# Performance work log

Hardware: AMD Instinct MI355X
Metric: run time of the kernel (lower is better)

The kernel has to match this reference:

```python
import jax, jax.numpy as jnp
import numpy as np

B = 4096
L = 15          # self.length
NINP = 256      # emb_size
NHID = 512      # hidden_size
VOCAB = 30005
TOPK = 10
K = 4 * TOPK + 2   # 42 actions
N_SPLIT = 2 * TOPK
N_STEP = 5      # num_edits
PAD = 30003


def _lstm_dir(x, Wih, Whh, b, reverse):
    # x: [T,B,D]; Wih: [4H,D]; Whh: [4H,H]; b: [4H] (b_ih+b_hh). PyTorch gate order i,f,g,o.
    Bsz, H = x.shape[1], Whh.shape[1]
    def step(carry, xt):
        h, c = carry
        z = xt @ Wih.T + h @ Whh.T + b
        i, f, g, o = jnp.split(z, 4, axis=-1)
        c = jax.nn.sigmoid(f) * c + jax.nn.sigmoid(i) * jnp.tanh(g)
        h = jax.nn.sigmoid(o) * jnp.tanh(c)
        return (h, c), h
    h0 = jnp.zeros((Bsz, H), x.dtype)
    _, ys = jax.lax.scan(step, (h0, h0), x, reverse=reverse)
    return ys  # [T,B,H], position-aligned for both directions


def bilstm(x, Wih0, Whh0, b0, Wih1, Whh1, b1):
    # x: [B,T,D] -> [B,T,2H]; 2-layer bidirectional, zero initial state (matches c0/h0 zeros).
    xt = jnp.swapaxes(x, 0, 1)
    for Wih, Whh, b in ((Wih0, Whh0, b0), (Wih1, Whh1, b1)):
        fw = _lstm_dir(xt, Wih[0], Whh[0], b[0], False)
        bw = _lstm_dir(xt, Wih[1], Whh[1], b[1], True)
        xt = jnp.concatenate([fw, bw], axis=-1)
    return jnp.swapaxes(xt, 0, 1)


def policy_step(st_1, length_t, pos, emb0, key_pos, rep_words, valid_id,
                emb_table, enc_table, Wih0, Whh0, b0, Wih1, Whh1, b1,
                del_vec, hold_vec, mlp_W, mlp_b, mlp1_W, mlp1_b):
    Bsz = st_1.shape[0]
    pos_row = jnp.zeros((L,), jnp.float32).at[pos].set(1.0)         # static pos
    pos_tensor = jnp.broadcast_to(pos_row[None, :, None], (Bsz, L, 1))
    embt = emb_table[st_1] * (1.0 - pos_tensor)
    x = jnp.concatenate([embt, emb0, pos_tensor], axis=2)            # [B,L,2*ninp+1]
    out = bilstm(x, Wih0, Whh0, b0, Wih1, Whh1, b1)                  # [B,L,2*nhid]
    pooled = out[:, pos, :]
    representation = jnp.concatenate(
        [pooled, key_pos[:, pos:pos + 1], jnp.broadcast_to(pos_row[None, :], (Bsz, L))], axis=1)
    # external encoder output is detached in the original
    word_emb = jax.lax.stop_gradient(enc_table[rep_words])           # [B,4*topk,ninp]
    emb2 = jnp.concatenate([word_emb,
                            jnp.broadcast_to(del_vec, (Bsz, 1, NINP)),
                            jnp.broadcast_to(hold_vec, (Bsz, 1, NINP))], axis=1)  # [B,K,ninp]
    onehot = jnp.broadcast_to(jnp.eye(K, dtype=jnp.float32)[None], (Bsz, K, K))
    emb2 = jnp.concatenate([emb2, onehot], axis=2)                   # [B,K,ninp+K]
    rep100 = representation @ mlp_W.T + mlp_b                        # [B,100]
    emb100 = emb2 @ mlp1_W.T + mlp1_b                                # [B,K,100]
    score = jnp.einsum('bkd,bd->bk', emb100, rep100)
    policy = jax.nn.softmax(score, axis=1)
    action = jnp.argmax(policy, axis=1, keepdims=True).astype(jnp.int32)  # eval mode
    pi = jnp.take_along_axis(policy, action, axis=1)                 # [B,1]

    rep_b = (action < N_SPLIT).astype(jnp.int32)
    replaceflag = rep_b * valid_id
    ins_b = ((action >= N_SPLIT) & (action < 2 * N_SPLIT)).astype(jnp.int32)
    insertflag = ins_b * valid_id * (length_t + ins_b <= 15).astype(jnp.int32)
    del_b = (action == 2 * N_SPLIT).astype(jnp.int32)
    deleteflag = del_b * valid_id * (length_t - del_b > 2).astype(jnp.int32)
    holdflag = 1 - replaceflag - insertflag - deleteflag

    action_words = jnp.take_along_axis(rep_words, jnp.clip(action, 0, N_SPLIT - 1), axis=1)  # [B,1]
    rep_seq = jnp.concatenate([action_words, st_1[:, pos + 1:]], axis=1)
    ins_seq = jnp.concatenate([action_words, st_1[:, pos:-1]], axis=1)
    padding = jnp.full((Bsz, 1), PAD, dtype=st_1.dtype)
    del_seq = jnp.concatenate([st_1[:, pos + 1:], padding], axis=1)
    hol_seq = st_1[:, pos:]
    new_tail = (rep_seq * replaceflag + ins_seq * insertflag
                + del_seq * deleteflag + hol_seq * holdflag)
    st = st_1.at[:, pos:].set(new_tail)
    length_tt = insertflag + length_t - deleteflag
    return st, pi, action.astype(jnp.float32), length_tt


def setup_inputs() -> dict:
    key = jax.random.key(0)
    ks = jax.random.split(key, 20)
    s = 0.05
    in0 = 2 * NINP + 1
    in1 = 2 * NHID
    inp = {
        'input_ids': jax.random.randint(ks[0], (B, L), 0, 30000, dtype=jnp.int32),
        'key_pos': jax.random.uniform(ks[1], (B, L), dtype=jnp.float32),
        'sequence_length': jax.random.randint(ks[2], (B, 1), 3, 16, dtype=jnp.int32),
        'rep_words_all': jax.random.randint(ks[3], (B, N_STEP, 4 * TOPK), 0, 30000, dtype=jnp.int32),
        'valid_id_all': jax.random.randint(ks[4], (B, N_STEP, 1), 0, 2, dtype=jnp.int32),
        'emb_table': jax.random.normal(ks[5], (VOCAB, NINP), jnp.float32) * s,
        'enc_table': jax.random.normal(ks[6], (VOCAB, NINP), jnp.float32) * s,
        'Wih0': jax.random.normal(ks[7], (2, 4 * NHID, in0), jnp.float32) * s,
        'Whh0': jax.random.normal(ks[8], (2, 4 * NHID, NHID), jnp.float32) * s,
        'b0': jax.random.normal(ks[9], (2, 4 * NHID), jnp.float32) * s,
        'Wih1': jax.random.normal(ks[10], (2, 4 * NHID, in1), jnp.float32) * s,
        'Whh1': jax.random.normal(ks[11], (2, 4 * NHID, NHID), jnp.float32) * s,
        'b1': jax.random.normal(ks[12], (2, 4 * NHID), jnp.float32) * s,
        'del_vec': jax.random.uniform(ks[13], (1, 1, NINP), dtype=jnp.float32),
        'hold_vec': jax.random.uniform(ks[14], (1, 1, NINP), dtype=jnp.float32),
        'mlp_W': jax.random.normal(ks[15], (100, 2 * NHID + 1 + L), jnp.float32) * s,
        'mlp_b': jnp.zeros((100,), jnp.float32),
        'mlp1_W': jax.random.normal(ks[16], (100, NINP + K), jnp.float32) * s,
        'mlp1_b': jnp.zeros((100,), jnp.float32),
    }
    return inp


def reference(input_ids, key_pos, sequence_length, rep_words_all, valid_id_all,
              emb_table, enc_table, Wih0, Whh0, b0, Wih1, Whh1, b1,
              del_vec, hold_vec, mlp_W, mlp_b, mlp1_W, mlp1_b):
    st = input_ids
    emb0 = emb_table[input_ids]            # embedding of s0, computed once
    length_t = sequence_length
    pis, acts = [], []
    for i in range(N_STEP):
        pos = i % (L - 3) + 2              # static per unrolled step
        st, pi, a, length_t = policy_step(
            st, length_t, pos, emb0, key_pos,
            rep_words_all[:, i, :], valid_id_all[:, i, :],
            emb_table, enc_table, Wih0, Whh0, b0, Wih1, Whh1, b1,
            del_vec, hold_vec, mlp_W, mlp_b, mlp1_W, mlp1_b)
        pis.append(pi)
        acts.append(a)
    pis = jnp.concatenate(pis, axis=1)     # [B,N_STEP]
    actions = jnp.concatenate(acts, axis=1)
    return pis, actions, st, length_t
```

## Files before the change

### kernel.cpp

```cpp
#include <hip/hip_runtime.h>

#define B_ 4096
#define L_ 15
#define NSTEP_ 5
#define VOC_ 30005
#define PAD_ 30003

typedef _Float16 f16;
typedef f16  f16x8 __attribute__((ext_vector_type(8)));
typedef float f32x16 __attribute__((ext_vector_type(16)));

__device__ __forceinline__ float sigf(float x){ return 1.0f/(1.0f+expf(-x)); }

#define MFMA_(d,a,b) d = __builtin_amdgcn_mfma_f32_32x32x16_f16(a,b,d,0,0,0)

struct RecParams {
  const f16 *A1h_0,*A1l_0,*A1h_1,*A1l_1;
  const f16 *A2h_0,*A2l_0,*A2h_1,*A2l_1;
  const f16 *Wfh_0,*Wfl_0,*Wfh_1,*Wfl_1;
  const float *bias_0,*bias_1;
  const f16 *embH,*embL;
  const int *st,*ids;
  float *c_0,*c_1,*h2_0,*h2_1;
  f16 *hh_0,*hl_0,*hh_1,*hl_1;
  int lda1, lda2, ldh, ldh2, k1p, k2p, first, gather, t_0, t_1, pos, b0c, act0, act1;
};

__device__ __forceinline__ int swz(int row, int s){
  int u = ((row&7)<<1) | s;
  return ((row>>3)<<8) + ((u ^ (u>>1))<<4);
}

__global__ __launch_bounds__(256,2) void rec_gemm(RecParams p){
  const int id  = blockIdx.x;
  const int ct4 = id & 15;
  const int dir = (id >> 4) & 1;
  if (!(dir ? p.act1 : p.act0)) return;
  const f16* A1h = dir ? p.A1h_1 : p.A1h_0;
  const f16* A1l = dir ? p.A1l_1 : p.A1l_0;
  const f16* A2h = dir ? p.A2h_1 : p.A2h_0;
  const f16* A2l = dir ? p.A2l_1 : p.A2l_0;
  const f16* Wfh = dir ? p.Wfh_1 : p.Wfh_0;
  const f16* Wfl = dir ? p.Wfl_1 : p.Wfl_0;
  const float* bias = dir ? p.bias_1 : p.bias_0;
  float* cbuf = dir ? p.c_1 : p.c_0;
  float* h2   = dir ? p.h2_1 : p.h2_0;
  f16* hhb = dir ? p.hh_1 : p.hh_0;
  f16* hlb = dir ? p.hl_1 : p.hl_0;
  const int tcur = dir ? p.t_1 : p.t_0;

  const int tid  = threadIdx.x;
  const int lane = tid & 63;
  const int w    = tid >> 6;
  const int mbase = (id >> 5) * 128;

  __shared__ union {
    float z[128*128];
    f16   stg[8][2048];
  } sm;

  f32x16 accM[2][2], accX[2][2];
#pragma unroll
  for (int i=0;i<2;i++)
#pragma unroll
    for (int j=0;j<2;j++)
#pragma unroll
      for (int r=0;r<16;r++){ accM[i][j][r]=0.f; accX[i][j][r]=0.f; }

  const int arow = (w&1)*64 + (lane&31);
  const int fs = lane>>5;
  const int aoff0 = swz(arow,    fs), aoff1 = swz(arow+32, fs);

  const int ct0 = ct4*4 + (w>>1)*2;
  const f16* WfhL = Wfh + (size_t)lane*8;
  const f16* WflL = Wfl + (size_t)lane*8;

  const int srow = tid >> 1, ss = tid & 1;
  const int sws = swz(srow, ss);
  const int ktot = p.k1p + p.k2p;

  int tokT=0, tokI=0, zflag=0;
  if (p.gather){
    int gb = p.b0c + mbase + srow;
    tokT = p.st [gb*L_ + tcur];
    tokI = p.ids[gb*L_ + tcur];
    zflag = (tcur == p.pos) ? 1 : 0;
  }

  f16x8 ra_h0, ra_l0, ra_h1, ra_l1;
  const f16x8 zero8 = {0,0,0,0,0,0,0,0};

  auto gload = [&](int ph){
    if (ph >= ktot) return;
    if (ph < p.k1p){
      if (p.gather){
        if (ph < 8){
          if (zflag){ ra_h0=zero8; ra_l0=zero8; ra_h1=zero8; ra_l1=zero8; }
          else {
            size_t base = (size_t)tokT*256 + ph*32 + ss*8;
            ra_h0 = *(const f16x8*)(p.embH + base);
            ra_l0 = *(const f16x8*)(p.embL + base);
            ra_h1 = *(const f16x8*)(p.embH + base + 16);
            ra_l1 = *(const f16x8*)(p.embL + base + 16);
          }
        } else if (ph < 16){
          size_t base = (size_t)tokI*256 + (ph-8)*32 + ss*8;
          ra_h0 = *(const f16x8*)(p.embH + base);
          ra_l0 = *(const f16x8*)(p.embL + base);
          ra_h1 = *(const f16x8*)(p.embH + base + 16);
          ra_l1 = *(const f16x8*)(p.embL + base + 16);
        } else {
          ra_h0 = zero8; ra_l0 = zero8; ra_h1 = zero8; ra_l1 = zero8;
          if (ss == 0) ra_h0[0] = zflag ? (f16)1.0f : (f16)0.0f;
        }
      } else {
        long base = (long)(mbase+srow)*p.lda1 + ph*32 + ss*8;
        ra_h0 = *(const f16x8*)(A1h + base);
        ra_l0 = *(const f16x8*)(A1l + base);
        ra_h1 = *(const f16x8*)(A1h + base + 16);
        ra_l1 = *(const f16x8*)(A1l + base + 16);
      }
    } else {
      long base = (long)(mbase+srow)*p.lda2 + (ph - p.k1p)*32 + ss*8;
      ra_h0 = *(const f16x8*)(A2h + base);
      ra_l0 = *(const f16x8*)(A2l + base);
      ra_h1 = *(const f16x8*)(A2h + base + 16);
      ra_l1 = *(const f16x8*)(A2l + base + 16);
    }
  };
  auto swrite = [&](int buf){
    *(f16x8*)((char*)sm.stg[buf*4+0] + sws) = ra_h0;
    *(f16x8*)((char*)sm.stg[buf*4+1] + sws) = ra_l0;
    *(f16x8*)((char*)sm.stg[buf*4+2] + sws) = ra_h1;
    *(f16x8*)((char*)sm.stg[buf*4+3] + sws) = ra_l1;
  };

  gload(0); swrite(0); gload(1);
  __syncthreads();

  for (int ph=0; ph<ktot; ++ph){
    const int cur = ph & 1;
    size_t base0 = ((size_t)(ph*2+0)*64 + ct0)*512;
    size_t base1 = ((size_t)(ph*2+1)*64 + ct0)*512;
    f16x8 rbh00 = *(const f16x8*)(WfhL + base0);
    f16x8 rbh01 = *(const f16x8*)(WfhL + base0 + 512);
    f16x8 rbl00 = *(const f16x8*)(WflL + base0);
    f16x8 rbl01 = *(const f16x8*)(WflL + base0 + 512);
    f16x8 rbh10 = *(const f16x8*)(WfhL + base1);
    f16x8 rbh11 = *(const f16x8*)(WfhL + base1 + 512);
    f16x8 rbl10 = *(const f16x8*)(WflL + base1);
    f16x8 rbl11 = *(const f16x8*)(WflL + base1 + 512);
    const char* s0h = (const char*)sm.stg[cur*4+0];
    const char* s0l = (const char*)sm.stg[cur*4+1];
    const char* s1h = (const char*)sm.stg[cur*4+2];
    const char* s1l = (const char*)sm.stg[cur*4+3];
    f16x8 a00h = *(const f16x8*)(s0h + aoff0);
    f16x8 a01h = *(const f16x8*)(s0h + aoff1);
    f16x8 a00l = *(const f16x8*)(s0l + aoff0);
    f16x8 a01l = *(const f16x8*)(s0l + aoff1);
    f16x8 a10h = *(const f16x8*)(s1h + aoff0);
    f16x8 a11h = *(const f16x8*)(s1h + aoff1);
    f16x8 a10l = *(const f16x8*)(s1l + aoff0);
    f16x8 a11l = *(const f16x8*)(s1l + aoff1);
    if (ph+1 < ktot){ swrite((ph+1)&1); gload(ph+2); }
    MFMA_(accM[0][0], a00h, rbh00); MFMA_(accX[0][0], a00h, rbl00); MFMA_(accX[0][0], a00l, rbh00);
    MFMA_(accM[1][0], a01h, rbh00); MFMA_(accX[1][0], a01h, rbl00); MFMA_(accX[1][0], a01l, rbh00);
    MFMA_(accM[0][1], a00h, rbh01); MFMA_(accX[0][1], a00h, rbl01); MFMA_(accX[0][1], a00l, rbh01);
    MFMA_(accM[1][1], a01h, rbh01); MFMA_(accX[1][1], a01h, rbl01); MFMA_(accX[1][1], a01l, rbh01);
    MFMA_(accM[0][0], a10h, rbh10); MFMA_(accX[0][0], a10h, rbl10); MFMA_(accX[0][0], a10l, rbh10);
    MFMA_(accM[1][0], a11h, rbh10); MFMA_(accX[1][0], a11h, rbl10); MFMA_(accX[1][0], a11l, rbh10);
    MFMA_(accM[0][1], a10h, rbh11); MFMA_(accX[0][1], a10h, rbl11); MFMA_(accX[0][1], a10l, rbh11);
    MFMA_(accM[1][1], a11h, rbh11); MFMA_(accX[1][1], a11h, rbl11); MFMA_(accX[1][1], a11l, rbh11);
    __syncthreads();
  }

#pragma unroll
  for (int tm=0;tm<2;tm++)
#pragma unroll
   for (int tn=0;tn<2;tn++){
    int lcol = (w>>1)*64 + tn*32 + (lane&31);
    float bv = bias[ct4*128 + lcol];
#pragma unroll
    for (int r=0;r<16;r++){
      int lrow = (w&1)*64 + tm*32 + (r&3) + 8*(r>>2) + 4*(lane>>5);
      sm.z[lrow*128 + lcol] = accM[tm][tn][r] + 0.000244140625f*accX[tm][tn][r] + bv;
    }
   }
  __syncthreads();

  const int nb = ct4*32;
#pragma unroll
  for (int it=0; it<16; ++it){
    int idx = it*256 + tid;
    int nq = idx & 31, row = idx >> 5;
    float4 g4 = *(const float4*)&sm.z[row*128 + nq*4];
    int m = mbase + row, n = nb + nq;
    float cp = p.first ? 0.f : cbuf[(size_t)m*512 + n];
    float cc = sigf(g4.y)*cp + sigf(g4.x)*tanhf(g4.z);
    float hv = sigf(g4.w)*tanhf(cc);
    cbuf[(size_t)m*512 + n] = cc;
    f16 hi = (f16)hv;
    f16 lo = (f16)((hv - (float)hi)*4096.0f);
    hhb[(size_t)m*p.ldh + n] = hi;
    hlb[(size_t)m*p.ldh + n] = lo;
    if (h2) h2[(size_t)m*p.ldh2 + n] = hv;
  }
}

__global__ void prep_w0(const float* Wih, const float* Whh, const float* b0,
                        f16* Wfh, f16* Wfl, float* bp){
  int gid = blockIdx.x*blockDim.x + threadIdx.x;
  const int PER_DIR = 66*64*64*8;
  if (gid >= 2*PER_DIR) return;
  int dir = gid / PER_DIR;
  int rem = gid % PER_DIR;
  int j = rem & 7, lane = (rem>>3)&63, ct = (rem>>9)&63, kt16 = rem>>15;
  int n4g = ct*32 + (lane&31);
  int n = n4g>>2, g = n4g&3;
  int srow = dir*2048 + g*512 + n;
  int k = kt16*16 + ((lane>>5)<<3) + j;
  float v;
  if (k < 513)       v = Wih[(size_t)srow*513 + k];
  else if (k < 544)  v = 0.f;
  else               v = Whh[(size_t)srow*512 + (k-544)];
  f16 hi = (f16)v;
  Wfh[gid] = hi;
  Wfl[gid] = (f16)((v - (float)hi)*4096.0f);
  if (kt16==0 && (lane>>5)==0 && j==0) bp[dir*2048 + n4g] = b0[srow];
}

__global__ void prep_w1(const float* Wih, const float* Whh, const float* b1,
                        f16* Wfh, f16* Wfl, float* bp){
  int gid = blockIdx.x*blockDim.x + threadIdx.x;
  const int PER_DIR = 96*64*64*8;
  if (gid >= 2*PER_DIR) return;
  int dir = gid / PER_DIR;
  int rem = gid % PER_DIR;
  int j = rem & 7, lane = (rem>>3)&63, ct = (rem>>9)&63, kt16 = rem>>15;
  int n4g = ct*32 + (lane&31);
  int n = n4g>>2, g = n4g&3;
  int srow = dir*2048 + g*512 + n;
  int k = kt16*16 + ((lane>>5)<<3) + j;
  float v;
  if (k < 1024) v = Wih[(size_t)srow*1024 + k];
  else          v = Whh[(size_t)srow*512 + (k-1024)];
  f16 hi = (f16)v;
  Wfh[gid] = hi;
  Wfl[gid] = (f16)((v - (float)hi)*4096.0f);
  if (kt16==0 && (lane>>5)==0 && j==0) bp[dir*2048 + n4g] = b1[srow];
}

__global__ void prep_emb(const float* emb, f16* eh, f16* el){
  int gid = blockIdx.x*blockDim.x + threadIdx.x;
  if (gid >= VOC_*256) return;
  float v = emb[gid];
  f16 hi = (f16)v;
  eh[gid] = hi;
  el[gid] = (f16)((v - (float)hi)*4096.0f);
}

__global__ void prep_mlpwt(const float* mW, float* wt){
  int gid = blockIdx.x*blockDim.x + threadIdx.x;
  if (gid >= 100*1040) return;
  int j = gid / 1040, k = gid % 1040;
  wt[k*100 + j] = mW[gid];
}

__global__ __launch_bounds__(128) void prep_encproj(const float* enc, const float* delv,
                        const float* holdv, const float* m1W, const float* m1b, float* ep){
  int r = blockIdx.x;
  __shared__ float row[256];
  const float* src = (r < VOC_) ? enc + (size_t)r*256 : (r == VOC_ ? delv : holdv);
  for (int i=threadIdx.x;i<256;i+=128) row[i]=src[i];
  __syncthreads();
  int j = threadIdx.x;
  if (j < 100){
    double s = (double)m1b[j];
    const float* wr = m1W + (size_t)j*298;
    for (int k=0;k<256;k++) s += (double)wr[k] * (double)row[k];
    ep[(size_t)r*100 + j] = (float)s;
  }
}

__global__ void init_st(const int* ids, const int* seqlen, int* st, int* len){
  int gid = blockIdx.x*blockDim.x + threadIdx.x;
  if (gid < B_*L_) st[gid] = ids[gid];
  if (gid < B_)    len[gid] = seqlen[gid];
}

__global__ void sentinel(float* out, float v){
  int gid = blockIdx.x*blockDim.x + threadIdx.x;
  if (gid < B_*NSTEP_) out[gid] = v;
}

__global__ __launch_bounds__(128) void score_update(
    const float* pooled, const float* keypos, const float* mWt, const float* mb,
    const float* ep, const float* m1W, const int* repw, const int* valid,
    int* st, int* len, float* outPis, float* outActs, int step, int pos, int b0){
  int b = blockIdx.x;
  int bg = b0 + b;
  __shared__ float rep[1040];
  __shared__ float r100[100];
  __shared__ double sc[42];
  int tid = threadIdx.x;
  for (int i=tid;i<1024;i+=128) rep[i] = pooled[(size_t)b*1024+i];
  if (tid < 16){
    if (tid == 0) rep[1024] = keypos[bg*L_+pos];
    else          rep[1024+tid] = ((tid-1)==pos) ? 1.f : 0.f;
  }
  __syncthreads();
  if (tid < 100){
    double s = (double)mb[tid];
    for (int k=0;k<1040;k++) s += (double)mWt[k*100+tid] * (double)rep[k];
    r100[tid] = (float)s;
  }
  __syncthreads();
  if (tid < 42){
    int row = (tid < 40) ? repw[((size_t)bg*NSTEP_+step)*40 + tid] : (VOC_ + (tid-40));
    const float* er = ep + (size_t)row*100;
    double s = 0.0;
    for (int j=0;j<100;j++) s += (double)er[j] * (double)r100[j];
    for (int j=0;j<100;j++) s += (double)m1W[j*298 + 256 + tid] * (double)r100[j];
    sc[tid] = s;
  }
  __syncthreads();
  if (tid == 0){
    double mx = sc[0]; int am = 0;
    for (int k=1;k<42;k++) if (sc[k] > mx){ mx = sc[k]; am = k; }
    double sum = 0.0;
    for (int k=0;k<42;k++) sum += exp(sc[k]-mx);
    float pi = (float)(1.0/sum);
    int vid = valid[bg*NSTEP_+step];
    int ln  = len[bg];
    int repb = (am < 20) ? 1 : 0;
    int insb = (am >= 20 && am < 40) ? 1 : 0;
    int delb = (am == 40) ? 1 : 0;
    int repf = repb*vid;
    int insf = insb*vid*(((ln+insb) <= 15) ? 1 : 0);
    int delf = delb*vid*(((ln-delb) >  2) ? 1 : 0);
    int T = L_ - pos;
    int tail[13];
    for (int j=0;j<T;j++) tail[j] = st[bg*L_+pos+j];
    int aw = repw[((size_t)bg*NSTEP_+step)*40 + (am < 20 ? am : 19)];
    for (int j=0;j<T;j++){
      int rv = (j==0) ? aw : tail[j];
      int iv = (j==0) ? aw : tail[j-1];
      int dv = (j < T-1) ? tail[j+1] : PAD_;
      int hv = tail[j];
      int nv = repf ? rv : (insf ? iv : (delf ? dv : hv));
      st[bg*L_+pos+j] = nv;
    }
    len[bg] = ln + insf - delf;
    outPis[bg*NSTEP_+step]  = pi;
    outActs[bg*NSTEP_+step] = (float)am;
  }
}

__global__ void finalize(const int* st, const int* len, float* out){
  int gid = blockIdx.x*blockDim.x + threadIdx.x;
  if (gid < B_*L_)            out[2*B_*NSTEP_ + gid] = (float)st[gid];
  else if (gid < B_*L_ + B_)  out[2*B_*NSTEP_ + B_*L_ + (gid - B_*L_)] = (float)len[gid - B_*L_];
}

extern "C" void kernel_launch(void* const* d_in, const int* in_sizes, int n_in,
                              void* d_out, int out_size, void* d_ws, size_t ws_size,
                              hipStream_t stream) {
  const int*   ids    = (const int*)  d_in[0];
  const float* keypos = (const float*)d_in[1];
  const int*   seqlen = (const int*)  d_in[2];
  const int*   repw   = (const int*)  d_in[3];
  const int*   valid  = (const int*)  d_in[4];
  const float* emb    = (const float*)d_in[5];
  const float* enc    = (const float*)d_in[6];
  const float* Wih0   = (const float*)d_in[7];
  const float* Whh0   = (const float*)d_in[8];
  const float* b0     = (const float*)d_in[9];
  const float* Wih1   = (const float*)d_in[10];
  const float* Whh1   = (const float*)d_in[11];
  const float* b1     = (const float*)d_in[12];
  const float* delv   = (const float*)d_in[13];
  const float* holdv  = (const float*)d_in[14];
  const float* mW     = (const float*)d_in[15];
  const float* mb     = (const float*)d_in[16];
  const float* m1W    = (const float*)d_in[17];
  const float* m1b    = (const float*)d_in[18];
  float* out = (float*)d_out;

  const size_t W0PD = (size_t)66*64*64*8;
  const size_t W1PD = (size_t)96*64*64*8;

  char* ws = (char*)d_ws;
  size_t off = 0;
  auto allocB = [&](size_t bytes) -> char* {
    char* pp = ws + off; off += (bytes + 255) & ~size_t(255); return pp;
  };
  f16*  Wf0h = (f16*)allocB(2*W0PD*2);
  f16*  Wf0l = (f16*)allocB(2*W0PD*2);
  f16*  Wf1h = (f16*)allocB(2*W1PD*2);
  f16*  Wf1l = (f16*)allocB(2*W1PD*2);
  float* bp0 = (float*)allocB(4096*4);
  float* bp1 = (float*)allocB(4096*4);
  f16*  embH = (f16*)allocB((size_t)VOC_*256*2);
  f16*  embL = (f16*)allocB((size_t)VOC_*256*2);
  float* mWt = (float*)allocB(104000*4);
  float* ep  = (float*)allocB((size_t)30007*100*4);
  int* stbuf  = (int*)allocB(B_*L_*4);
  int* lenbuf = (int*)allocB(B_*4);
  size_t fixedB = off;

  const int cands[6] = {4096, 2048, 1024, 512, 256, 128};
  int Bc = 0;
  for (int ci=0; ci<6; ++ci){
    size_t c = cands[ci];
    size_t chunkB = c*(size_t)(15*1024*2*2 + 4*512*2*2 + 2*512*4 + 2*512*4 + 1024*4) + 8*256;
    if (fixedB + chunkB <= ws_size){ Bc = (int)c; break; }
  }
  if (!Bc){
    float code = 100000.0f + (float)(ws_size >> 20);
    sentinel<<<(B_*NSTEP_+255)/256,256,0,stream>>>(out, code);
    return;
  }
  f16* o0h = (f16*)allocB((size_t)L_*Bc*1024*2);
  f16* o0l = (f16*)allocB((size_t)L_*Bc*1024*2);
  f16* h1h = (f16*)allocB((size_t)4*Bc*512*2);
  f16* h1l = (f16*)allocB((size_t)4*Bc*512*2);
  float* c0 = (float*)allocB((size_t)2*Bc*512*4);
  float* c1 = (float*)allocB((size_t)2*Bc*512*4);
  float* pooled = (float*)allocB((size_t)Bc*1024*4);

  prep_w0<<<(int)((2*W0PD+255)/256),256,0,stream>>>(Wih0, Whh0, b0, Wf0h, Wf0l, bp0);
  prep_w1<<<(int)((2*W1PD+255)/256),256,0,stream>>>(Wih1, Whh1, b1, Wf1h, Wf1l, bp1);
  prep_emb<<<(VOC_*256+255)/256,256,0,stream>>>(emb, embH, embL);
  prep_mlpwt<<<(100*1040+255)/256,256,0,stream>>>(mW, mWt);
  prep_encproj<<<30007,128,0,stream>>>(enc, delv, holdv, m1W, m1b, ep);
  init_st<<<(B_*L_+255)/256,256,0,stream>>>(ids, seqlen, stbuf, lenbuf);

  const int nblk = (Bc/128) * 32;

  for (int b0c=0; b0c<B_; b0c+=Bc){
    for (int step=0; step<NSTEP_; ++step){
      int pos = step + 2;

      for (int ts=0; ts<L_; ++ts){
        int tf = ts, tb = 14-ts;
        RecParams p{};
        p.gather = 1; p.t_0 = tf; p.t_1 = tb; p.pos = pos; p.b0c = b0c;
        p.embH = embH; p.embL = embL; p.st = stbuf; p.ids = ids;
        p.k1p = 17; p.k2p = ts ? 16 : 0;
        size_t of0 = (size_t)(ts?tf-1:0)*Bc*1024;
        size_t of1 = (size_t)(ts?tb+1:0)*Bc*1024 + (ts?512:0);
        p.A2h_0 = o0h + of0;  p.A2l_0 = o0l + of0;
        p.A2h_1 = o0h + of1;  p.A2l_1 = o0l + of1;
        p.lda2 = 1024;
        p.Wfh_0 = Wf0h;        p.Wfl_0 = Wf0l;
        p.Wfh_1 = Wf0h + W0PD; p.Wfl_1 = Wf0l + W0PD;
        p.bias_0 = bp0; p.bias_1 = bp0 + 2048;
        p.c_0 = c0; p.c_1 = c0 + (size_t)Bc*512;
        p.hh_0 = o0h + (size_t)tf*Bc*1024;       p.hl_0 = o0l + (size_t)tf*Bc*1024;
        p.hh_1 = o0h + (size_t)tb*Bc*1024 + 512; p.hl_1 = o0l + (size_t)tb*Bc*1024 + 512;
        p.ldh = 1024;
        p.h2_0 = nullptr; p.h2_1 = nullptr; p.ldh2 = 1024;
        p.first = (ts==0); p.act0 = 1; p.act1 = 1;
        rec_gemm<<<dim3(nblk),256,0,stream>>>(p);
      }

      int nL1 = L_ - pos;
      for (int ts=0; ts<nL1; ++ts){
        RecParams p{};
        int tf = ts, tb = 14-ts;
        int parR = (ts-1)&1, parW = ts&1;
        p.gather = 0;
        p.A1h_0 = o0h + (size_t)tf*Bc*1024;  p.A1l_0 = o0l + (size_t)tf*Bc*1024;
        p.A1h_1 = o0h + (size_t)tb*Bc*1024;  p.A1l_1 = o0l + (size_t)tb*Bc*1024;
        p.lda1 = 1024; p.k1p = 32;
        p.k2p  = ts ? 16 : 0;
        size_t r0 = (size_t)(0*2 + (ts?parR:0))*Bc*512;
        size_t r1 = (size_t)(1*2 + (ts?parR:0))*Bc*512;
        p.A2h_0 = h1h + r0; p.A2l_0 = h1l + r0;
        p.A2h_1 = h1h + r1; p.A2l_1 = h1l + r1;
        p.lda2 = 512;
        p.Wfh_0 = Wf1h;        p.Wfl_0 = Wf1l;
        p.Wfh_1 = Wf1h + W1PD; p.Wfl_1 = Wf1l + W1PD;
        p.bias_0 = bp1; p.bias_1 = bp1 + 2048;
        p.c_0 = c1; p.c_1 = c1 + (size_t)Bc*512;
        size_t w0 = (size_t)(0*2 + parW)*Bc*512;
        size_t w1 = (size_t)(1*2 + parW)*Bc*512;
        p.hh_0 = h1h + w0; p.hl_0 = h1l + w0;
        p.hh_1 = h1h + w1; p.hl_1 = h1l + w1;
        p.ldh = 512;
        p.h2_0 = (ts == pos)    ? pooled        : nullptr;
        p.h2_1 = (ts == 14-pos) ? (pooled+512)  : nullptr;
        p.ldh2 = 1024;
        p.first = (ts==0);
        p.act0 = (ts <= pos) ? 1 : 0; p.act1 = 1;
        rec_gemm<<<dim3(nblk),256,0,stream>>>(p);
      }

      score_update<<<Bc,128,0,stream>>>(pooled, keypos, mWt, mb, ep, m1W, repw, valid,
                                        stbuf, lenbuf, out, out + B_*NSTEP_, step, pos, b0c);
    }
  }
  finalize<<<(B_*L_+B_+255)/256,256,0,stream>>>(stbuf, lenbuf, out);
}
```

Measured before the change: 20.20 ms.

## Widen rec_gemm tiles to 128x256 with 512-thread blocks and split epilogue

The recurrent GEMM block grows from 256 to 512 threads and its output tile from 128 to 256 gate columns, so each staged A tile in shared memory is reused by twice as many columns. The grid becomes 2D (column tile by direction, times batch tile), which halves the block count. Staging loads are spread across twice as many threads, and the epilogue writes the gate tile through shared memory in two halves so the shared-memory size stays the same. The cost is fewer blocks, larger blocks and more barriers in the epilogue, which may hurt occupancy and latency hiding.

New measurement: 18.89 ms. -6.5%, faster.

```diff
diff --git a/kernel.cpp b/kernel.cpp
--- a/kernel.cpp
+++ b/kernel.cpp
@@ -31,10 +31,10 @@
   return ((row>>3)<<8) + ((u ^ (u>>1))<<4);
 }
 
-__global__ __launch_bounds__(256,2) void rec_gemm(RecParams p){
-  const int id  = blockIdx.x;
-  const int ct4 = id & 15;
-  const int dir = (id >> 4) & 1;
+__global__ __launch_bounds__(512,2) void rec_gemm(RecParams p){
+  const int bxe = blockIdx.x;
+  const int ct8 = bxe & 7;
+  const int dir = bxe >> 3;
   if (!(dir ? p.act1 : p.act0)) return;
   const f16* A1h = dir ? p.A1h_1 : p.A1h_0;
   const f16* A1l = dir ? p.A1l_1 : p.A1l_0;
@@ -52,7 +52,7 @@
   const int tid  = threadIdx.x;
   const int lane = tid & 63;
   const int w    = tid >> 6;
-  const int mbase = (id >> 5) * 128;
+  const int mbase = blockIdx.y*128;
 
   __shared__ union {
     float z[128*128];
@@ -71,12 +71,14 @@
   const int fs = lane>>5;
   const int aoff0 = swz(arow,    fs), aoff1 = swz(arow+32, fs);
 
-  const int ct0 = ct4*4 + (w>>1)*2;
+  const int ct0 = ct8*8 + (w>>1)*2;
   const f16* WfhL = Wfh + (size_t)lane*8;
   const f16* WflL = Wfl + (size_t)lane*8;
 
-  const int srow = tid >> 1, ss = tid & 1;
+  const int u = tid & 255, pr = tid >> 8;
+  const int srow = u >> 1, ss = u & 1;
   const int sws = swz(srow, ss);
+  const int kph = pr*16 + ss*8;
   const int ktot = p.k1p + p.k2p;
 
   int tokT=0, tokI=0, zflag=0;
@@ -87,7 +89,7 @@
     zflag = (tcur == p.pos) ? 1 : 0;
   }
 
-  f16x8 ra_h0, ra_l0, ra_h1, ra_l1;
+  f16x8 ra_h, ra_l;
   const f16x8 zero8 = {0,0,0,0,0,0,0,0};
 
   auto gload = [&](int ph){
@@ -95,44 +97,34 @@
     if (ph < p.k1p){
       if (p.gather){
         if (ph < 8){
-          if (zflag){ ra_h0=zero8; ra_l0=zero8; ra_h1=zero8; ra_l1=zero8; }
+          if (zflag){ ra_h=zero8; ra_l=zero8; }
           else {
-            size_t base = (size_t)tokT*256 + ph*32 + ss*8;
-            ra_h0 = *(const f16x8*)(p.embH + base);
-            ra_l0 = *(const f16x8*)(p.embL + base);
-            ra_h1 = *(const f16x8*)(p.embH + base + 16);
-            ra_l1 = *(const f16x8*)(p.embL + base + 16);
+            size_t base = (size_t)tokT*256 + ph*32 + kph;
+            ra_h = *(const f16x8*)(p.embH + base);
+            ra_l = *(const f16x8*)(p.embL + base);
           }
         } else if (ph < 16){
-          size_t base = (size_t)tokI*256 + (ph-8)*32 + ss*8;
-          ra_h0 = *(const f16x8*)(p.embH + base);
-          ra_l0 = *(const f16x8*)(p.embL + base);
-          ra_h1 = *(const f16x8*)(p.embH + base + 16);
-          ra_l1 = *(const f16x8*)(p.embL + base + 16);
+          size_t base = (size_t)tokI*256 + (ph-8)*32 + kph;
+          ra_h = *(const f16x8*)(p.embH + base);
+          ra_l = *(const f16x8*)(p.embL + base);
         } else {
-          ra_h0 = zero8; ra_l0 = zero8; ra_h1 = zero8; ra_l1 = zero8;
-          if (ss == 0) ra_h0[0] = zflag ? (f16)1.0f : (f16)0.0f;
+          ra_h = zero8; ra_l = zero8;
+          if (kph == 0) ra_h[0] = zflag ? (f16)1.0f : (f16)0.0f;
         }
       } else {
-        long base = (long)(mbase+srow)*p.lda1 + ph*32 + ss*8;
-        ra_h0 = *(const f16x8*)(A1h + base);
-        ra_l0 = *(const f16x8*)(A1l + base);
-        ra_h1 = *(const f16x8*)(A1h + base + 16);
-        ra_l1 = *(const f16x8*)(A1l + base + 16);
+        long base = (long)(mbase+srow)*p.lda1 + ph*32 + kph;
+        ra_h = *(const f16x8*)(A1h + base);
+        ra_l = *(const f16x8*)(A1l + base);
       }
     } else {
-      long base = (long)(mbase+srow)*p.lda2 + (ph - p.k1p)*32 + ss*8;
-      ra_h0 = *(const f16x8*)(A2h + base);
-      ra_l0 = *(const f16x8*)(A2l + base);
-      ra_h1 = *(const f16x8*)(A2h + base + 16);
-      ra_l1 = *(const f16x8*)(A2l + base + 16);
+      long base = (long)(mbase+srow)*p.lda2 + (ph - p.k1p)*32 + kph;
+      ra_h = *(const f16x8*)(A2h + base);
+      ra_l = *(const f16x8*)(A2l + base);
     }
   };
   auto swrite = [&](int buf){
-    *(f16x8*)((char*)sm.stg[buf*4+0] + sws) = ra_h0;
-    *(f16x8*)((char*)sm.stg[buf*4+1] + sws) = ra_l0;
-    *(f16x8*)((char*)sm.stg[buf*4+2] + sws) = ra_h1;
-    *(f16x8*)((char*)sm.stg[buf*4+3] + sws) = ra_l1;
+    *(f16x8*)((char*)sm.stg[buf*4 + pr*2 + 0] + sws) = ra_h;
+    *(f16x8*)((char*)sm.stg[buf*4 + pr*2 + 1] + sws) = ra_l;
   };
 
   gload(0); swrite(0); gload(1);
@@ -174,36 +166,41 @@
     __syncthreads();
   }
 
-#pragma unroll
-  for (int tm=0;tm<2;tm++)
-#pragma unroll
-   for (int tn=0;tn<2;tn++){
-    int lcol = (w>>1)*64 + tn*32 + (lane&31);
-    float bv = bias[ct4*128 + lcol];
-#pragma unroll
-    for (int r=0;r<16;r++){
-      int lrow = (w&1)*64 + tm*32 + (r&3) + 8*(r>>2) + 4*(lane>>5);
-      sm.z[lrow*128 + lcol] = accM[tm][tn][r] + 0.000244140625f*accX[tm][tn][r] + bv;
+  const int cq = w >> 1;
+  for (int hf=0; hf<2; ++hf){
+    if ((cq>>1) == hf){
+#pragma unroll
+      for (int tm=0;tm<2;tm++)
+#pragma unroll
+       for (int tn=0;tn<2;tn++){
+        int lcol = (cq&1)*64 + tn*32 + (lane&31);
+        float bv = bias[ct8*256 + hf*128 + lcol];
+#pragma unroll
+        for (int r=0;r<16;r++){
+          int lrow = (w&1)*64 + tm*32 + (r&3) + 8*(r>>2) + 4*(lane>>5);
+          sm.z[lrow*128 + lcol] = accM[tm][tn][r] + 0.000244140625f*accX[tm][tn][r] + bv;
+        }
+       }
     }
-   }
-  __syncthreads();
-
-  const int nb = ct4*32;
-#pragma unroll
-  for (int it=0; it<16; ++it){
-    int idx = it*256 + tid;
-    int nq = idx & 31, row = idx >> 5;
-    float4 g4 = *(const float4*)&sm.z[row*128 + nq*4];
-    int m = mbase + row, n = nb + nq;
-    float cp = p.first ? 0.f : cbuf[(size_t)m*512 + n];
-    float cc = sigf(g4.y)*cp + sigf(g4.x)*tanhf(g4.z);
-    float hv = sigf(g4.w)*tanhf(cc);
-    cbuf[(size_t)m*512 + n] = cc;
-    f16 hi = (f16)hv;
-    f16 lo = (f16)((hv - (float)hi)*4096.0f);
-    hhb[(size_t)m*p.ldh + n] = hi;
-    hlb[(size_t)m*p.ldh + n] = lo;
-    if (h2) h2[(size_t)m*p.ldh2 + n] = hv;
+    __syncthreads();
+    const int nb = ct8*64 + hf*32;
+#pragma unroll
+    for (int it=0; it<8; ++it){
+      int idx = it*512 + tid;
+      int nq = idx & 31, row = idx >> 5;
+      float4 g4 = *(const float4*)&sm.z[row*128 + nq*4];
+      int m = mbase + row, n = nb + nq;
+      float cp = p.first ? 0.f : cbuf[(size_t)m*512 + n];
+      float cc = sigf(g4.y)*cp + sigf(g4.x)*tanhf(g4.z);
+      float hv = sigf(g4.w)*tanhf(cc);
+      cbuf[(size_t)m*512 + n] = cc;
+      f16 hi = (f16)hv;
+      f16 lo = (f16)((hv - (float)hi)*4096.0f);
+      hhb[(size_t)m*p.ldh + n] = hi;
+      hlb[(size_t)m*p.ldh + n] = lo;
+      if (h2) h2[(size_t)m*p.ldh2 + n] = hv;
+    }
+    __syncthreads();
   }
 }
 
@@ -435,8 +432,6 @@
   prep_encproj<<<30007,128,0,stream>>>(enc, delv, holdv, m1W, m1b, ep);
   init_st<<<(B_*L_+255)/256,256,0,stream>>>(ids, seqlen, stbuf, lenbuf);
 
-  const int nblk = (Bc/128) * 32;
-
   for (int b0c=0; b0c<B_; b0c+=Bc){
     for (int step=0; step<NSTEP_; ++step){
       int pos = step + 2;
@@ -461,7 +456,7 @@
         p.ldh = 1024;
         p.h2_0 = nullptr; p.h2_1 = nullptr; p.ldh2 = 1024;
         p.first = (ts==0); p.act0 = 1; p.act1 = 1;
-        rec_gemm<<<dim3(nblk),256,0,stream>>>(p);
+        rec_gemm<<<dim3(16,Bc/128),512,0,stream>>>(p);
       }
 
       int nL1 = L_ - pos;
@@ -493,7 +488,7 @@
         p.ldh2 = 1024;
         p.first = (ts==0);
         p.act0 = (ts <= pos) ? 1 : 0; p.act1 = 1;
-        rec_gemm<<<dim3(nblk),256,0,stream>>>(p);
+        rec_gemm<<<dim3(16,Bc/128),512,0,stream>>>(p);
       }
 
       score_update<<<Bc,128,0,stream>>>(pooled, keypos, mWt, mb, ep, m1W, repw, valid,
```
